# Performance work log

Hardware: AMD Instinct MI355X
Metric: run time of the kernel (lower is better)

Reference implementation:

```python
import jax, jax.numpy as jnp
import numpy as np

KERNEL = 5  # init kwarg kernel_size


def _extract_patches_same(x, k):
    # tf.image.extract_patches, stride 1, rate 1, SAME padding.
    # Returns [B, h, w, k*k, C] with patch positions row-major (di, dj).
    B, h, w, C = x.shape
    pad = k // 2
    xp = jnp.pad(x, ((0, 0), (pad, pad), (pad, pad), (0, 0)))
    return jnp.stack(
        [xp[:, di:di + h, dj:dj + w, :] for di in range(k) for dj in range(k)],
        axis=3,
    )


def _nearest_idx(out_size, in_size):
    # TF v2 nearest resize (half-pixel centers): src = floor((dst+0.5)*in/out)
    idx = jnp.floor((jnp.arange(out_size) + 0.5) * (in_size / out_size))
    return jnp.clip(idx.astype(jnp.int32), 0, in_size - 1)


def setup_inputs() -> dict:
    key = jax.random.key(0)
    kf, km = jax.random.split(key)
    features = jax.random.normal(kf, (2, 64, 64, 128), dtype=jnp.float32)
    masks = jax.random.normal(km, (2, 128, 128, 25), dtype=jnp.float32)
    return {"features": features, "masks": masks}


def reference(features, masks):
    k = KERNEL
    k2 = k * k
    B, h, w, C = features.shape
    H, W, Mc = masks.shape[1], masks.shape[2], masks.shape[3]
    G = Mc // k2  # group_size
    Cg = C // G

    # im2col patch extraction at low resolution: [B, h, w, k2, C]
    patches = _extract_patches_same(features, k)

    # nearest-neighbor upsample of patch tensor to mask resolution
    ri = _nearest_idx(H, h)
    ci = _nearest_idx(W, w)
    fp = patches[:, ri][:, :, ci]  # [B, H, W, k2, C]
    fp = fp.reshape(B, H, W, k2, G, Cg)

    # per-pixel softmax over kernel window, grouped reassembly
    m = jax.nn.softmax(masks.reshape(B, H, W, G, k2), axis=-1)
    out = jnp.einsum('bhwkgc,bhwgk->bhwgc', fp, m)  # [B, H, W, G, Cg]
    return out.reshape(B, H, W, C)
```

## Files before the change

### kernel.cpp

```cpp
#include <hip/hip_runtime.h>
#include <math.h>


#define K  5
#define K2 25

typedef float v4f __attribute__((ext_vector_type(4)));

__global__ __launch_bounds__(256) void carafe_quad_kernel(
    const float* __restrict__ feat,
    const float* __restrict__ masks,
    float* __restrict__ out)
{
    __shared__ v4f wq[8][K2];

    const int group = threadIdx.x >> 5;
    const int lane  = threadIdx.x & 31;

    const int q   = blockIdx.x * 8 + group;
    const int b   = q >> 12;
    const int rem = q & 4095;
    const int r   = rem >> 6;
    const int c   = rem & 63;

    const int pix00 = ((b * 128 + 2 * r) * 128 + 2 * c);
    const int pixofs[4] = {0, 1, 128, 129};

    float w[4];
    #pragma unroll
    for (int p = 0; p < 4; ++p) {
        const int pix = pix00 + pixofs[p];
        float mv = (lane < K2) ? masks[(size_t)pix * K2 + lane] : -INFINITY;
        float mx = mv;
        #pragma unroll
        for (int off = 16; off >= 1; off >>= 1)
            mx = fmaxf(mx, __shfl_xor(mx, off, 32));
        float e = (lane < K2) ? __expf(mv - mx) : 0.0f;
        float s = e;
        #pragma unroll
        for (int off = 16; off >= 1; off >>= 1)
            s += __shfl_xor(s, off, 32);
        w[p] = e / s;
    }
    if (lane < K2) {
        float* dst = (float*)&wq[group][lane];
        dst[0] = w[0]; dst[1] = w[1]; dst[2] = w[2]; dst[3] = w[3];
    }
    __syncthreads();

    v4f acc0 = 0.f, acc1 = 0.f, acc2 = 0.f, acc3 = 0.f;
    const v4f* featv = (const v4f*)feat;
    const size_t fbase = (size_t)b * (64 * 64 * 32);

    #pragma unroll
    for (int j = 0; j < K2; ++j) {
        const int di = j / K;
        const int dj = j % K;
        const int rr = r + di - 2;
        const int cc = c + dj - 2;
        if ((unsigned)rr < 64u && (unsigned)cc < 64u) {
            const v4f wj = wq[group][j];
            const v4f f  = featv[fbase + (size_t)(rr * 64 + cc) * 32 + lane];
            acc0 += f * wj.x;
            acc1 += f * wj.y;
            acc2 += f * wj.z;
            acc3 += f * wj.w;
        }
    }

    v4f* outv = (v4f*)out;
    outv[(size_t)(pix00 +   0) * 32 + lane] = acc0;
    outv[(size_t)(pix00 +   1) * 32 + lane] = acc1;
    outv[(size_t)(pix00 + 128) * 32 + lane] = acc2;
    outv[(size_t)(pix00 + 129) * 32 + lane] = acc3;
}

extern "C" void kernel_launch(void* const* d_in, const int* in_sizes, int n_in,
                              void* d_out, int out_size, void* d_ws, size_t ws_size,
                              hipStream_t stream) {
    const float* feat  = (const float*)d_in[0];
    const float* masks = (const float*)d_in[1];
    float* out = (float*)d_out;

    dim3 grid((2 * 64 * 64) / 8), block(256);
    carafe_quad_kernel<<<grid, block, 0, stream>>>(feat, masks, out);
}
```

Baseline: 70.54 us.

## Stage shared feature tile in LDS for cooperative reuse across quads

Each block now loads a 5x12 halo tile of low-res features into shared memory once, and all 8 quads in the row segment read their 5x5 windows from it instead of fetching each from global memory. The tile loads are issued into registers before the softmax so their latency overlaps that math, and are written to LDS afterwards. This cuts redundant global/L2 feature reads, at the cost of about 30KB of LDS per block, which can limit occupancy. Zero-padding is baked into the tile, which removes the per-tap bounds checks.

New measurement: 68.70 us. 1.03x faster.

```diff
diff --git a/kernel.cpp b/kernel.cpp
--- a/kernel.cpp
+++ b/kernel.cpp
@@ -2,28 +2,53 @@
 #include <math.h>
 
 
-#define K  5
-#define K2 25
+#define K   5
+#define K2  25
+#define QPB 8
+#define TW  (QPB + K - 1)
+#define TH  K
+#define NPIX (TH * TW)
 
 typedef float v4f __attribute__((ext_vector_type(4)));
 
-__global__ __launch_bounds__(256) void carafe_quad_kernel(
+__global__ __launch_bounds__(256) void carafe_tile_kernel(
     const float* __restrict__ feat,
     const float* __restrict__ masks,
     float* __restrict__ out)
 {
-    __shared__ v4f wq[8][K2];
+    __shared__ v4f tile[TH][TW][32];
+    __shared__ v4f wq[QPB][K2];
 
-    const int group = threadIdx.x >> 5;
-    const int lane  = threadIdx.x & 31;
+    const int tid   = threadIdx.x;
+    const int group = tid >> 5;
+    const int lane  = tid & 31;
 
-    const int q   = blockIdx.x * 8 + group;
-    const int b   = q >> 12;
-    const int rem = q & 4095;
+    const int q0  = blockIdx.x * QPB;
+    const int b   = q0 >> 12;
+    const int rem = q0 & 4095;
     const int r   = rem >> 6;
-    const int c   = rem & 63;
+    const int c0  = rem & 63;
 
-    const int pix00 = ((b * 128 + 2 * r) * 128 + 2 * c);
+    const v4f* featv = (const v4f*)feat;
+    const size_t fbase = (size_t)b * (64 * 64 * 32);
+
+    v4f stg[8];
+    #pragma unroll
+    for (int i = 0; i < 8; ++i) {
+        const int p = group + i * 8;
+        v4f v = 0.f;
+        if (p < NPIX) {
+            const int row = p / TW;
+            const int col = p - row * TW;
+            const int gr  = r  - 2 + row;
+            const int gc  = c0 - 2 + col;
+            if ((unsigned)gr < 64u && (unsigned)gc < 64u)
+                v = featv[fbase + (size_t)(gr * 64 + gc) * 32 + lane];
+        }
+        stg[i] = v;
+    }
+
+    const int pix00 = ((b * 128 + 2 * r) * 128 + 2 * (c0 + group));
     const int pixofs[4] = {0, 1, 128, 129};
 
     float w[4];
@@ -42,6 +67,13 @@
             s += __shfl_xor(s, off, 32);
         w[p] = e / s;
     }
+
+    #pragma unroll
+    for (int i = 0; i < 8; ++i) {
+        const int p = group + i * 8;
+        if (p < NPIX)
+            ((v4f*)tile)[p * 32 + lane] = stg[i];
+    }
     if (lane < K2) {
         float* dst = (float*)&wq[group][lane];
         dst[0] = w[0]; dst[1] = w[1]; dst[2] = w[2]; dst[3] = w[3];
@@ -49,23 +81,16 @@
     __syncthreads();
 
     v4f acc0 = 0.f, acc1 = 0.f, acc2 = 0.f, acc3 = 0.f;
-    const v4f* featv = (const v4f*)feat;
-    const size_t fbase = (size_t)b * (64 * 64 * 32);
-
     #pragma unroll
     for (int j = 0; j < K2; ++j) {
         const int di = j / K;
         const int dj = j % K;
-        const int rr = r + di - 2;
-        const int cc = c + dj - 2;
-        if ((unsigned)rr < 64u && (unsigned)cc < 64u) {
-            const v4f wj = wq[group][j];
-            const v4f f  = featv[fbase + (size_t)(rr * 64 + cc) * 32 + lane];
-            acc0 += f * wj.x;
-            acc1 += f * wj.y;
-            acc2 += f * wj.z;
-            acc3 += f * wj.w;
-        }
+        const v4f wj = wq[group][j];
+        const v4f f  = tile[di][group + dj][lane];
+        acc0 += f * wj.x;
+        acc1 += f * wj.y;
+        acc2 += f * wj.z;
+        acc3 += f * wj.w;
     }
 
     v4f* outv = (v4f*)out;
@@ -82,6 +107,6 @@
     const float* masks = (const float*)d_in[1];
     float* out = (float*)d_out;
 
-    dim3 grid((2 * 64 * 64) / 8), block(256);
-    carafe_quad_kernel<<<grid, block, 0, stream>>>(feat, masks, out);
+    dim3 grid((2 * 64 * 64) / QPB), block(256);
+    carafe_tile_kernel<<<grid, block, 0, stream>>>(feat, masks, out);
 }
```

## Map one wave64 per quad, broadcast softmax weights via readlane instead of LDS

Applied to the files above, without the earlier changes.

Each 64-lane wave now handles one low-res pixel's 2x2 output quad. Each half-wave computes the softmax for one output row, and each lane covers 2 channels instead of 4 in a 32-lane group. The weights reach all lanes through readlane broadcasts, which removes the shared-memory staging and __syncthreads. The change also remaps block indices into an interleaved order and adds a launch-bounds occupancy hint. The trade is narrower per-lane loads and scalar readlane work for every tap, in exchange for dropping LDS and the barrier.

Measured after the change: 70.34 us. About the same (-0.3%).

```diff
diff --git a/kernel.cpp b/kernel.cpp
--- a/kernel.cpp
+++ b/kernel.cpp
@@ -5,74 +5,80 @@
 #define K  5
 #define K2 25
 
-typedef float v4f __attribute__((ext_vector_type(4)));
+typedef float v2f __attribute__((ext_vector_type(2)));
 
-__global__ __launch_bounds__(256) void carafe_quad_kernel(
+__device__ __forceinline__ float readlane_f32(float v, int l) {
+    return __builtin_bit_cast(float,
+        __builtin_amdgcn_readlane(__builtin_bit_cast(int, v), l));
+}
+
+__global__ __launch_bounds__(256, 6) void carafe_wave_kernel(
     const float* __restrict__ feat,
     const float* __restrict__ masks,
     float* __restrict__ out)
 {
-    __shared__ v4f wq[8][K2];
+    const int bid = blockIdx.x;
+    const int wg  = (bid & 7) * (2048 >> 3) + (bid >> 3);
 
-    const int group = threadIdx.x >> 5;
-    const int lane  = threadIdx.x & 31;
+    const int wid  = __builtin_amdgcn_readfirstlane(threadIdx.x >> 6);
+    const int lane = threadIdx.x & 63;
+    const int half = lane >> 5;
+    const int l32  = lane & 31;
 
-    const int q   = blockIdx.x * 8 + group;
+    const int q   = wg * 4 + wid;
     const int b   = q >> 12;
     const int rem = q & 4095;
     const int r   = rem >> 6;
     const int c   = rem & 63;
 
     const int pix00 = ((b * 128 + 2 * r) * 128 + 2 * c);
-    const int pixofs[4] = {0, 1, 128, 129};
 
-    float w[4];
+    float w[2];
     #pragma unroll
-    for (int p = 0; p < 4; ++p) {
-        const int pix = pix00 + pixofs[p];
-        float mv = (lane < K2) ? masks[(size_t)pix * K2 + lane] : -INFINITY;
+    for (int rnd = 0; rnd < 2; ++rnd) {
+        const int pix = pix00 + half * 128 + rnd;
+        float mv = (l32 < K2) ? masks[(size_t)pix * K2 + l32] : -INFINITY;
         float mx = mv;
         #pragma unroll
         for (int off = 16; off >= 1; off >>= 1)
             mx = fmaxf(mx, __shfl_xor(mx, off, 32));
-        float e = (lane < K2) ? __expf(mv - mx) : 0.0f;
+        float e = (l32 < K2) ? __expf(mv - mx) : 0.0f;
         float s = e;
         #pragma unroll
         for (int off = 16; off >= 1; off >>= 1)
             s += __shfl_xor(s, off, 32);
-        w[p] = e / s;
+        w[rnd] = e / s;
     }
-    if (lane < K2) {
-        float* dst = (float*)&wq[group][lane];
-        dst[0] = w[0]; dst[1] = w[1]; dst[2] = w[2]; dst[3] = w[3];
-    }
-    __syncthreads();
 
-    v4f acc0 = 0.f, acc1 = 0.f, acc2 = 0.f, acc3 = 0.f;
-    const v4f* featv = (const v4f*)feat;
-    const size_t fbase = (size_t)b * (64 * 64 * 32);
+    v2f acc0 = 0.f, acc1 = 0.f, acc2 = 0.f, acc3 = 0.f;
+    const float* fb = feat + (size_t)b * (64 * 64 * 128) + lane * 2;
 
     #pragma unroll
-    for (int j = 0; j < K2; ++j) {
-        const int di = j / K;
-        const int dj = j % K;
+    for (int di = 0; di < K; ++di) {
         const int rr = r + di - 2;
-        const int cc = c + dj - 2;
-        if ((unsigned)rr < 64u && (unsigned)cc < 64u) {
-            const v4f wj = wq[group][j];
-            const v4f f  = featv[fbase + (size_t)(rr * 64 + cc) * 32 + lane];
-            acc0 += f * wj.x;
-            acc1 += f * wj.y;
-            acc2 += f * wj.z;
-            acc3 += f * wj.w;
+        if ((unsigned)rr >= 64u) continue;
+        #pragma unroll
+        for (int dj = 0; dj < K; ++dj) {
+            const int cc = c + dj - 2;
+            if ((unsigned)cc >= 64u) continue;
+            const int j = di * K + dj;
+            const float w0 = readlane_f32(w[0], j);
+            const float w1 = readlane_f32(w[1], j);
+            const float w2 = readlane_f32(w[0], j + 32);
+            const float w3 = readlane_f32(w[1], j + 32);
+            const v2f f = *(const v2f*)(fb + (size_t)(rr * 64 + cc) * 128);
+            acc0 += f * w0;
+            acc1 += f * w1;
+            acc2 += f * w2;
+            acc3 += f * w3;
         }
     }
 
-    v4f* outv = (v4f*)out;
-    outv[(size_t)(pix00 +   0) * 32 + lane] = acc0;
-    outv[(size_t)(pix00 +   1) * 32 + lane] = acc1;
-    outv[(size_t)(pix00 + 128) * 32 + lane] = acc2;
-    outv[(size_t)(pix00 + 129) * 32 + lane] = acc3;
+    float* ob = out + (size_t)pix00 * 128 + lane * 2;
+    *(v2f*)(ob + 0)               = acc0;
+    *(v2f*)(ob + 128)             = acc1;
+    *(v2f*)(ob + 128 * 128)       = acc2;
+    *(v2f*)(ob + 128 * 128 + 128) = acc3;
 }
 
 extern "C" void kernel_launch(void* const* d_in, const int* in_sizes, int n_in,
@@ -82,6 +88,6 @@
     const float* masks = (const float*)d_in[1];
     float* out = (float*)d_out;
 
-    dim3 grid((2 * 64 * 64) / 8), block(256);
-    carafe_quad_kernel<<<grid, block, 0, stream>>>(feat, masks, out);
+    dim3 grid(8192 / 4), block(256);
+    carafe_wave_kernel<<<grid, block, 0, stream>>>(feat, masks, out);
 }
```
